# Kernel optimization log

Hardware: AMD Instinct MI355X
Metric: run time of the kernel (lower is better)

## Reference

```python
import jax, jax.numpy as jnp
import numpy as np


def _rgcn(x, src, dst, et, basis, comp, root, bias):
    # Basis-decomposed RGCNConv (PyG semantics): per-relation mean aggregation
    # over incoming edges + root transform + bias.
    N = x.shape[0]
    R = comp.shape[0]
    W = jnp.einsum('rb,bio->rio', comp, basis)          # [R, in, out]
    xr = jnp.einsum('ni,rio->rno', x, W)                 # [R, N, out]
    msg = xr[et, src]                                    # [E, out] gather per edge
    seg = dst * R + et                                   # (target, relation) segment id
    cnt = jax.ops.segment_sum(jnp.ones(et.shape, x.dtype), seg, num_segments=N * R)
    norm = 1.0 / jnp.maximum(cnt, 1.0)                   # mean per (dst, relation)
    msg = msg * norm[seg][:, None]
    agg = jax.ops.segment_sum(msg, dst, num_segments=N)  # scatter-add to targets
    return agg + x @ root + bias


def setup_inputs() -> dict:
    key = jax.random.key(0)
    ks = jax.random.split(key, 20)
    N, E, R, B, F, D, C, NB = 100000, 1600000, 5, 512, 4, 32, 5, 2
    s = 0.1
    inp = {
        'x': jax.random.normal(ks[0], (N, F), jnp.float32),
        'edge_index': jax.random.randint(ks[1], (2, E), 0, N, dtype=jnp.int32),
        'edge_type': jax.random.randint(ks[2], (E,), 0, R, dtype=jnp.int32),
        'start_nodes': jax.random.randint(ks[3], (B,), 0, N, dtype=jnp.int32),
        # layer 0: in=F, out=D
        'basis0': jax.random.normal(ks[4], (NB, F, D), jnp.float32) * s,
        'comp0': jax.random.normal(ks[5], (R, NB), jnp.float32) * s,
        'root0': jax.random.normal(ks[6], (F, D), jnp.float32) * s,
        'bias0': jax.random.normal(ks[7], (D,), jnp.float32) * s,
        # layers 1..3: in=out=D, stacked
        'basis': jax.random.normal(ks[8], (3, NB, D, D), jnp.float32) * s,
        'comp': jax.random.normal(ks[9], (3, R, NB), jnp.float32) * s,
        'root': jax.random.normal(ks[10], (3, D, D), jnp.float32) * s,
        'bias': jax.random.normal(ks[11], (3, D), jnp.float32) * s,
        # MLP head: sum(latent_dim)=128 -> 128 -> C
        'lin1_w': jax.random.normal(ks[12], (4 * D, 128), jnp.float32) * s,
        'lin1_b': jax.random.normal(ks[13], (128,), jnp.float32) * s,
        'lin2_w': jax.random.normal(ks[14], (128, C), jnp.float32) * s,
        'lin2_b': jax.random.normal(ks[15], (C,), jnp.float32) * s,
    }
    return inp


def reference(x, edge_index, edge_type, start_nodes, basis0, comp0, root0, bias0,
              basis, comp, root, bias, lin1_w, lin1_b, lin2_w, lin2_b):
    src, dst = edge_index[0], edge_index[1]
    h = jnp.tanh(_rgcn(x, src, dst, edge_type, basis0, comp0, root0, bias0))
    states = [h]
    for l in range(basis.shape[0]):
        h = jnp.tanh(_rgcn(h, src, dst, edge_type, basis[l], comp[l], root[l], bias[l]))
        states.append(h)
    concat = jnp.concatenate(states, axis=1)             # [N, 128]
    # Per-graph readout: the walk's degenerate n_walks=1 branch, i.e. the
    # start (user) node's concatenated state (sequential backtracking walk
    # replaced by its deterministic initialization path; eval mode, no dropout).
    acc = concat[start_nodes]                            # [B, 128]
    h1 = jax.nn.relu(acc @ lin1_w + lin1_b)
    logits = h1 @ lin2_w + lin2_b
    return jax.nn.log_softmax(logits, axis=-1)
```

## Files before the change

### kernel.cpp

```cpp
#include <hip/hip_runtime.h>
#include <cstdint>

#define N_NODES 100000
#define N_EDGES 1600000
#define R_REL   5
#define NBASIS  2
#define B_START 512
#define NBUCK   256
#define BUCK_SZ 391
#define EPB     6250
#define STAGE_CAP 7000

typedef __attribute__((ext_vector_type(8))) short short8;
typedef __attribute__((ext_vector_type(4))) float f32x4;
typedef _Float16 half8 __attribute__((ext_vector_type(8)));
typedef unsigned uint32x2 __attribute__((ext_vector_type(2)));
typedef unsigned uint32x4 __attribute__((ext_vector_type(4)));

__device__ __forceinline__ unsigned short f2bf(float f) {
    unsigned u = __float_as_uint(f);
    unsigned r = (u + 0x7FFF + ((u >> 16) & 1)) >> 16;
    return (unsigned short)r;
}
__device__ __forceinline__ float bf2f(unsigned short u) {
    return __uint_as_float(((unsigned)u) << 16);
}
__device__ __forceinline__ unsigned short f2h(float f) {
    _Float16 h = (_Float16)f;
    return __builtin_bit_cast(unsigned short, h);
}


__global__ __launch_bounds__(256) void k_cntb(
    const int* __restrict__ ei, int* __restrict__ bhist) {
    __shared__ int lh[NBUCK];
    int tid = threadIdx.x;
    lh[tid] = 0;
    __syncthreads();
    int base = blockIdx.x * EPB;
    for (int j = tid; j < EPB; j += 256) {
        int dst = ei[N_EDGES + base + j];
        atomicAdd(&lh[dst / BUCK_SZ], 1);
    }
    __syncthreads();
    bhist[blockIdx.x * NBUCK + tid] = lh[tid];
}

__global__ __launch_bounds__(256) void k_colscan(
    int* __restrict__ bhist, int* __restrict__ colsum) {
    __shared__ int s[256];
    int b = blockIdx.x, i = threadIdx.x;
    int v = bhist[i * NBUCK + b];
    s[i] = v;
    __syncthreads();
    for (int o = 1; o < 256; o <<= 1) {
        int t = (i >= o) ? s[i - o] : 0;
        __syncthreads();
        s[i] += t;
        __syncthreads();
    }
    bhist[i * NBUCK + b] = s[i] - v;
    if (i == 255) colsum[b] = s[255];
}

__global__ __launch_bounds__(256) void k_tiny(
    const int* __restrict__ colsum, int* __restrict__ bbase) {
    __shared__ int s[256];
    int i = threadIdx.x;
    int v = colsum[i];
    s[i] = v;
    __syncthreads();
    for (int o = 1; o < 256; o <<= 1) {
        int t = (i >= o) ? s[i - o] : 0;
        __syncthreads();
        s[i] += t;
        __syncthreads();
    }
    bbase[i] = s[i] - v;
    if (i == 255) bbase[NBUCK] = s[255];
}

__global__ __launch_bounds__(256) void k_scat(
    const int* __restrict__ ei, const int* __restrict__ et,
    const int* __restrict__ bhist, const int* __restrict__ bbase,
    int* __restrict__ arena) {
    __shared__ int lc[NBUCK];
    int tid = threadIdx.x;
    lc[tid] = bhist[blockIdx.x * NBUCK + tid] + bbase[tid];
    __syncthreads();
    int base = blockIdx.x * EPB;
    for (int j = tid; j < EPB; j += 256) {
        int e   = base + j;
        int src = ei[e];
        int dst = ei[N_EDGES + e];
        int t   = et[e];
        int bk  = dst / BUCK_SZ;
        int dl  = dst - bk * BUCK_SZ;
        int pos = atomicAdd(&lc[bk], 1);
        arena[pos] = src | (t << 17) | (dl << 20);
    }
}

__global__ __launch_bounds__(256) void k_build(
    const int* __restrict__ arena, const int* __restrict__ bbase,
    int* __restrict__ off, int* __restrict__ pk_m, float* __restrict__ nv5,
    unsigned* __restrict__ degpk) {
    __shared__ int deg5[BUCK_SZ * R_REL];
    __shared__ int loff[BUCK_SZ + 1];
    __shared__ int cur5[BUCK_SZ * R_REL];
    __shared__ int stg[STAGE_CAP];
    __shared__ int tsum[256];
    int b = blockIdx.x, tid = threadIdx.x;
    int base = bbase[b], end = bbase[b + 1];
    int count = end - base;
    for (int i = tid; i < BUCK_SZ * R_REL; i += 256) deg5[i] = 0;
    __syncthreads();
    for (int i = tid; i < count; i += 256) {
        int r  = arena[base + i];
        int dl = ((unsigned)r) >> 20;
        int t  = (r >> 17) & 7;
        atomicAdd(&deg5[dl * R_REL + t], 1);
    }
    __syncthreads();
    for (int dl = tid; dl < BUCK_SZ; dl += 256) {
        loff[dl] = deg5[dl * R_REL + 0] + deg5[dl * R_REL + 1] +
                   deg5[dl * R_REL + 2] + deg5[dl * R_REL + 3] +
                   deg5[dl * R_REL + 4];
    }
    __syncthreads();
    int d0 = 2 * tid, d1 = 2 * tid + 1;
    int va = (d0 < BUCK_SZ) ? loff[d0] : 0;
    int vb = (d1 < BUCK_SZ) ? loff[d1] : 0;
    tsum[tid] = va + vb;
    __syncthreads();
    for (int o = 1; o < 256; o <<= 1) {
        int v = (tid >= o) ? tsum[tid - o] : 0;
        __syncthreads();
        tsum[tid] += v;
        __syncthreads();
    }
    int pre = tsum[tid] - (va + vb);
    if (d0 < BUCK_SZ) loff[d0] = pre;
    if (d1 < BUCK_SZ) loff[d1] = pre + va;
    __syncthreads();
    for (int dl = tid; dl < BUCK_SZ; dl += 256) {
        int nn = b * BUCK_SZ + dl;
        int run = loff[dl];
        unsigned dp = 0;
#pragma unroll
        for (int t = 0; t < R_REL; t++) {
            cur5[dl * R_REL + t] = run;
            int c = deg5[dl * R_REL + t];
            run += c;
            int cc = c > 63 ? 63 : c;
            dp |= ((unsigned)cc) << (6 * t);
        }
        if (nn < N_NODES) {
            off[nn]   = base + loff[dl];
            degpk[nn] = dp;
#pragma unroll
            for (int t = 0; t < R_REL; t++) {
                int c = deg5[dl * R_REL + t];
                nv5[nn * R_REL + t] = 1.0f / (float)(c > 0 ? c : 1);
            }
        }
    }
    if (b == NBUCK - 1 && tid == 0) off[N_NODES] = N_EDGES;
    __syncthreads();
    for (int i = tid; i < count; i += 256) {
        int r  = arena[base + i];
        int dl = ((unsigned)r) >> 20;
        int t  = (r >> 17) & 7;
        int rk = atomicAdd(&cur5[dl * R_REL + t], 1);
        if (rk < STAGE_CAP) stg[rk] = r;
    }
    __syncthreads();
    for (int i = tid; i < count; i += 256) {
        int r = stg[i < STAGE_CAP ? i : STAGE_CAP - 1];
        pk_m[base + i] = r & 0x1FFFF;
    }
}


__global__ __launch_bounds__(256) void k_wprep(
    const float* __restrict__ basis, const float* __restrict__ comp,
    const float* __restrict__ root,  const float* __restrict__ basis0,
    const float* __restrict__ comp0, const float* __restrict__ root0,
    unsigned short* __restrict__ wfh, unsigned short* __restrict__ wfr,
    unsigned short* __restrict__ wf0) {
    __shared__ float lw[5120];
    int tid = threadIdx.x;
    int l = blockIdx.x;
    if (l < 3) {
        for (int idx = tid; idx < 5120; idx += 256) {
            int r = idx >> 10, rem = idx & 1023, i = rem >> 5, o = rem & 31;
            lw[idx] = comp[l * 10 + r * 2 + 0] * basis[l * 2048 + i * 32 + o]
                    + comp[l * 10 + r * 2 + 1] * basis[l * 2048 + 1024 + i * 32 + o];
        }
        __syncthreads();
        for (int idx = tid; idx < 5120; idx += 256) {
            int ot = idx / 2560, rem = idx % 2560;
            int s = rem >> 9, ln = (rem >> 3) & 63, j = idx & 7;
            int o = ot * 16 + (ln & 15), kk = (ln >> 4) * 8 + j;
            wfh[l * 5120 + idx] = f2h(lw[s * 1024 + kk * 32 + o]);
        }
        for (int idx = tid; idx < 2048; idx += 256) {
            int ot = idx >> 10, s = (idx >> 9) & 1, ln = (idx >> 3) & 63, j = idx & 7;
            int o = ot * 16 + (ln & 15), kk = (ln >> 4) * 8 + j;
            float val = root[l * 1024 + kk * 32 + o];
            unsigned short hi = f2bf(val);
            wfr[l * 2048 + idx] = s ? f2bf(val - bf2f(hi)) : hi;
        }
    } else {
        for (int idx = tid; idx < 1024; idx += 256) {
            int k = idx >> 5, o = idx & 31;
            float val = 0.f;
            if (k < 20) {
                int r = k >> 2, i = k & 3;
                val = comp0[r * 2 + 0] * basis0[i * 32 + o]
                    + comp0[r * 2 + 1] * basis0[128 + i * 32 + o];
            } else if (k < 24) val = root0[(k - 20) * 32 + o];
            lw[idx] = val;
        }
        __syncthreads();
        for (int idx = tid; idx < 1024; idx += 256) {
            int ot = idx >> 9, ln = (idx >> 3) & 63, j = idx & 7;
            int o = ot * 16 + (ln & 15), kk = (ln >> 4) * 8 + j;
            wf0[idx] = f2h(lw[kk * 32 + o]);
        }
    }
}


__global__ __launch_bounds__(256) void k_cvt0(
    const float* __restrict__ x, unsigned short* __restrict__ hb0) {
    int n = blockIdx.x * 256 + threadIdx.x;
    if (n >= N_NODES) return;
    float4 xv = *(const float4*)(x + (size_t)n * 4);
    unsigned short h0 = f2bf(xv.x), h1 = f2bf(xv.y), h2 = f2bf(xv.z), h3 = f2bf(xv.w);
    unsigned long long ph = (unsigned long long)h0 | ((unsigned long long)h1 << 16)
                          | ((unsigned long long)h2 << 32) | ((unsigned long long)h3 << 48);
    *(unsigned long long*)(hb0 + (size_t)n * 4) = ph;
}


__global__ __launch_bounds__(256) void k_gath32(
    const unsigned short* __restrict__ hb, const int* __restrict__ pk_m,
    const float* __restrict__ nv5, const unsigned* __restrict__ degpk,
    const int* __restrict__ off, unsigned short* __restrict__ agg) {
    int tid = threadIdx.x;
    int n = blockIdx.x * 8 + (tid >> 5);
    int lane32 = tid & 31;
    int s = lane32 >> 2;
    int cpos = lane32 & 3;

    int e0 = off[n];
    unsigned dp = degpk[n];
    int c0 = dp & 63, c1 = (dp >> 6) & 63, c2 = (dp >> 12) & 63,
        c3 = (dp >> 18) & 63, c4 = (dp >> 24) & 63;
    int cnt = s == 0 ? c0 : s == 1 ? c1 : s == 2 ? c2 : s == 3 ? c3
            : s == 4 ? c4 : 0;
    int start = (s > 0 ? c0 : 0) + (s > 1 ? c1 : 0) + (s > 2 ? c2 : 0)
              + (s > 3 ? c3 : 0);
    float nv = (s < R_REL) ? nv5[n * R_REL + s] : 0.f;

    const uint32x4* __restrict__ hb4 = (const uint32x4*)hb;
    float a0 = 0.f, a1 = 0.f, a2 = 0.f, a3 = 0.f;
    float a4 = 0.f, a5 = 0.f, a6 = 0.f, a7 = 0.f;
    int base = e0 + start;
    int pb = base < N_EDGES ? base : N_EDGES - 1;
    int mcur = __builtin_nontemporal_load(pk_m + pb);
    for (int k = 0; k < cnt; ++k) {
        int kn = k + 1 < cnt ? k + 1 : cnt - 1;
        int mnxt = __builtin_nontemporal_load(pk_m + base + kn);
        uint32x4 u = hb4[(size_t)mcur * 4 + cpos];
        a0 += nv * __uint_as_float(u.x << 16);
        a1 += nv * __uint_as_float(u.x & 0xFFFF0000u);
        a2 += nv * __uint_as_float(u.y << 16);
        a3 += nv * __uint_as_float(u.y & 0xFFFF0000u);
        a4 += nv * __uint_as_float(u.z << 16);
        a5 += nv * __uint_as_float(u.z & 0xFFFF0000u);
        a6 += nv * __uint_as_float(u.w << 16);
        a7 += nv * __uint_as_float(u.w & 0xFFFF0000u);
        mcur = mnxt;
    }
    if (s < R_REL) {
        uint32x4 pk;
        pk.x = (unsigned)f2h(a0) | ((unsigned)f2h(a1) << 16);
        pk.y = (unsigned)f2h(a2) | ((unsigned)f2h(a3) << 16);
        pk.z = (unsigned)f2h(a4) | ((unsigned)f2h(a5) << 16);
        pk.w = (unsigned)f2h(a6) | ((unsigned)f2h(a7) << 16);
        __builtin_nontemporal_store(pk,
            (uint32x4*)(agg + (size_t)n * 160 + s * 32 + cpos * 8));
    }
}


__global__ __launch_bounds__(256) void k_gath0(
    const unsigned short* __restrict__ hb0, const float* __restrict__ x,
    const int* __restrict__ pk_m, const float* __restrict__ nv5,
    const unsigned* __restrict__ degpk, const int* __restrict__ off,
    unsigned short* __restrict__ a0v) {
    int tid = threadIdx.x;
    int n = blockIdx.x * 32 + (tid >> 3);
    int s = tid & 7;

    int e0 = off[n];
    unsigned dp = degpk[n];
    int c0 = dp & 63, c1 = (dp >> 6) & 63, c2 = (dp >> 12) & 63,
        c3 = (dp >> 18) & 63, c4 = (dp >> 24) & 63;
    int cnt = s == 0 ? c0 : s == 1 ? c1 : s == 2 ? c2 : s == 3 ? c3
            : s == 4 ? c4 : 0;
    int start = (s > 0 ? c0 : 0) + (s > 1 ? c1 : 0) + (s > 2 ? c2 : 0)
              + (s > 3 ? c3 : 0);
    float nv = (s < R_REL) ? nv5[n * R_REL + s] : 0.f;

    const uint32x2* __restrict__ hb2 = (const uint32x2*)hb0;
    float a0 = 0.f, a1 = 0.f, a2 = 0.f, a3 = 0.f;
    int base = e0 + start;
    int pb = base < N_EDGES ? base : N_EDGES - 1;
    int mcur = __builtin_nontemporal_load(pk_m + pb);
    for (int k = 0; k < cnt; ++k) {
        int kn = k + 1 < cnt ? k + 1 : cnt - 1;
        int mnxt = __builtin_nontemporal_load(pk_m + base + kn);
        uint32x2 u = hb2[mcur];
        a0 += nv * __uint_as_float(u.x << 16);
        a1 += nv * __uint_as_float(u.x & 0xFFFF0000u);
        a2 += nv * __uint_as_float(u.y << 16);
        a3 += nv * __uint_as_float(u.y & 0xFFFF0000u);
        mcur = mnxt;
    }
    if (s < R_REL) {
        uint32x2 pk;
        pk.x = (unsigned)f2h(a0) | ((unsigned)f2h(a1) << 16);
        pk.y = (unsigned)f2h(a2) | ((unsigned)f2h(a3) << 16);
        __builtin_nontemporal_store(pk,
            (uint32x2*)(a0v + (size_t)n * 32 + s * 4));
    } else if (s == 5) {
        float4 xv = *(const float4*)(x + (size_t)n * 4);
        uint32x2 pk;
        pk.x = (unsigned)f2h(xv.x) | ((unsigned)f2h(xv.y) << 16);
        pk.y = (unsigned)f2h(xv.z) | ((unsigned)f2h(xv.w) << 16);
        __builtin_nontemporal_store(pk,
            (uint32x2*)(a0v + (size_t)n * 32 + 20));
    } else {
        uint32x2 z;
        z.x = 0u; z.y = 0u;
        __builtin_nontemporal_store(z,
            (uint32x2*)(a0v + (size_t)n * 32 + 24 + (s - 6) * 4));
    }
}


__global__ __launch_bounds__(256) void k_gemm(
    const unsigned short* __restrict__ agg, const unsigned short* __restrict__ hbin,
    const unsigned short* __restrict__ wfhl, const unsigned short* __restrict__ wfrl,
    const float* __restrict__ biasL, float* __restrict__ h,
    unsigned short* __restrict__ hbout) {
    int tid = threadIdx.x;
    int wid = tid >> 6, lane = tid & 63;
    int tile = blockIdx.x * 4 + wid;
    if (tile >= N_NODES / 16) return;
    int n0 = tile * 16;
    int row = lane & 15, kg = lane >> 4;
    const half8* ar = (const half8*)(agg + (size_t)(n0 + row) * 160 + kg * 8);
    const half8* wh = (const half8*)wfhl;
    const short8* wr = (const short8*)wfrl;
    short8 hbf = *(const short8*)(hbin + (size_t)(n0 + row) * 32 + kg * 8);
    f32x4 c0 = {0.f, 0.f, 0.f, 0.f}, c1 = {0.f, 0.f, 0.f, 0.f};
#pragma unroll
    for (int s = 0; s < 5; s++) {
        half8 a = __builtin_nontemporal_load(&ar[s * 4]);
        c0 = __builtin_amdgcn_mfma_f32_16x16x32_f16(a, wh[s * 64 + lane], c0, 0, 0, 0);
        c1 = __builtin_amdgcn_mfma_f32_16x16x32_f16(a, wh[320 + s * 64 + lane], c1, 0, 0, 0);
    }
    c0 = __builtin_amdgcn_mfma_f32_16x16x32_bf16(hbf, wr[lane], c0, 0, 0, 0);
    c0 = __builtin_amdgcn_mfma_f32_16x16x32_bf16(hbf, wr[64 + lane], c0, 0, 0, 0);
    c1 = __builtin_amdgcn_mfma_f32_16x16x32_bf16(hbf, wr[128 + lane], c1, 0, 0, 0);
    c1 = __builtin_amdgcn_mfma_f32_16x16x32_bf16(hbf, wr[192 + lane], c1, 0, 0, 0);
    float b0 = biasL[row], b1 = biasL[16 + row];
#pragma unroll
    for (int i = 0; i < 4; i++) {
        int n = n0 + kg * 4 + i;
        float t0 = tanhf(c0[i] + b0);
        float t1 = tanhf(c1[i] + b1);
        h[(size_t)n * 32 + row]      = t0;
        h[(size_t)n * 32 + 16 + row] = t1;
        hbout[(size_t)n * 32 + row]      = f2bf(t0);
        hbout[(size_t)n * 32 + 16 + row] = f2bf(t1);
    }
}

__global__ __launch_bounds__(256) void k_gemm0(
    const unsigned short* __restrict__ a0v, const unsigned short* __restrict__ wf0,
    const float* __restrict__ biasL, float* __restrict__ h,
    unsigned short* __restrict__ hbout) {
    int tid = threadIdx.x;
    int wid = tid >> 6, lane = tid & 63;
    int tile = blockIdx.x * 4 + wid;
    if (tile >= N_NODES / 16) return;
    int n0 = tile * 16;
    int row = lane & 15, kg = lane >> 4;
    half8 a = *(const half8*)(a0v + (size_t)(n0 + row) * 32 + kg * 8);
    const half8* wv = (const half8*)wf0;
    f32x4 c0 = {0.f, 0.f, 0.f, 0.f}, c1 = {0.f, 0.f, 0.f, 0.f};
    c0 = __builtin_amdgcn_mfma_f32_16x16x32_f16(a, wv[lane], c0, 0, 0, 0);
    c1 = __builtin_amdgcn_mfma_f32_16x16x32_f16(a, wv[64 + lane], c1, 0, 0, 0);
    float b0 = biasL[row], b1 = biasL[16 + row];
#pragma unroll
    for (int i = 0; i < 4; i++) {
        int n = n0 + kg * 4 + i;
        float t0 = tanhf(c0[i] + b0);
        float t1 = tanhf(c1[i] + b1);
        h[(size_t)n * 32 + row]      = t0;
        h[(size_t)n * 32 + 16 + row] = t1;
        hbout[(size_t)n * 32 + row]      = f2bf(t0);
        hbout[(size_t)n * 32 + 16 + row] = f2bf(t1);
    }
}


__global__ void k_save(const float* __restrict__ h, const int* __restrict__ start,
                       float* __restrict__ sav) {
    int t = blockIdx.x * blockDim.x + threadIdx.x;
    if (t < B_START * 32) {
        int b = t >> 5, ln = t & 31;
        sav[t] = h[(size_t)start[b] * 32 + ln];
    }
}

__global__ __launch_bounds__(128) void k_mlp(
    const float* __restrict__ sav, const float* __restrict__ w1,
    const float* __restrict__ b1, const float* __restrict__ w2,
    const float* __restrict__ b2, float* __restrict__ out) {
    __shared__ float cvec[128];
    __shared__ float hb[128];
    __shared__ float lg[8];
    int b = blockIdx.x, t = threadIdx.x;
    cvec[t] = sav[(t >> 5) * (B_START * 32) + b * 32 + (t & 31)];
    __syncthreads();
    float a = b1[t];
#pragma unroll 8
    for (int k = 0; k < 128; k++) a += cvec[k] * w1[k * 128 + t];
    hb[t] = fmaxf(a, 0.f);
    __syncthreads();
    if (t < 5) {
        float a2 = b2[t];
        for (int k = 0; k < 128; k++) a2 += hb[k] * w2[k * 5 + t];
        lg[t] = a2;
    }
    __syncthreads();
    if (t < 5) {
        float m = lg[0];
        for (int j = 1; j < 5; j++) m = fmaxf(m, lg[j]);
        float s = 0.f;
        for (int j = 0; j < 5; j++) s += expf(lg[j] - m);
        out[b * 5 + t] = lg[t] - m - logf(s);
    }
}


extern "C" void kernel_launch(void* const* d_in, const int* in_sizes, int n_in,
                              void* d_out, int out_size, void* d_ws, size_t ws_size,
                              hipStream_t stream) {
    const float* x      = (const float*)d_in[0];
    const int*   ei     = (const int*)d_in[1];
    const int*   etype  = (const int*)d_in[2];
    const int*   start  = (const int*)d_in[3];
    const float* basis0 = (const float*)d_in[4];
    const float* comp0  = (const float*)d_in[5];
    const float* root0  = (const float*)d_in[6];
    const float* bias0  = (const float*)d_in[7];
    const float* basis  = (const float*)d_in[8];
    const float* comp   = (const float*)d_in[9];
    const float* root   = (const float*)d_in[10];
    const float* bias   = (const float*)d_in[11];
    const float* w1     = (const float*)d_in[12];
    const float* b1     = (const float*)d_in[13];
    const float* w2     = (const float*)d_in[14];
    const float* b2     = (const float*)d_in[15];
    float* out = (float*)d_out;

    char* p = (char*)d_ws;
    auto alloc = [&](size_t bytes) -> void* {
        void* r = (void*)p;
        p += (bytes + 255) & ~(size_t)255;
        return r;
    };
    int*            bhist  = (int*)alloc((size_t)NBUCK * NBUCK * 4);
    int*            colsum = (int*)alloc(NBUCK * 4);
    int*            bbase  = (int*)alloc((NBUCK + 1) * 4);
    int*            arena  = (int*)alloc((size_t)N_EDGES * 4);
    int*            off    = (int*)alloc((N_NODES + 1) * 4);
    int*            pk_m   = (int*)alloc((size_t)N_EDGES * 4);
    float*          nv5    = (float*)alloc((size_t)N_NODES * R_REL * 4);
    unsigned*       degpk  = (unsigned*)alloc((size_t)N_NODES * 4);
    float*          h      = (float*)alloc((size_t)N_NODES * 32 * 4);
    unsigned short* hbuf   = (unsigned short*)alloc((size_t)(N_NODES + 64) * 32 * 2);
    unsigned short* hb0    = (unsigned short*)alloc((size_t)N_NODES * 4 * 2);
    unsigned short* a0v    = (unsigned short*)alloc((size_t)(N_NODES + 64) * 32 * 2);
    unsigned short* agg    = (unsigned short*)alloc((size_t)(N_NODES + 64) * 160 * 2);
    unsigned short* wfh    = (unsigned short*)alloc((size_t)3 * 5120 * 2);
    unsigned short* wfr    = (unsigned short*)alloc((size_t)3 * 2048 * 2);
    unsigned short* wf0    = (unsigned short*)alloc((size_t)1024 * 2);
    float*          sav    = (float*)alloc(4 * B_START * 32 * 4);

    k_cntb<<<NBUCK, 256, 0, stream>>>(ei, bhist);
    k_colscan<<<NBUCK, 256, 0, stream>>>(bhist, colsum);
    k_tiny<<<1, 256, 0, stream>>>(colsum, bbase);
    k_scat<<<NBUCK, 256, 0, stream>>>(ei, etype, bhist, bbase, arena);
    k_build<<<NBUCK, 256, 0, stream>>>(arena, bbase, off, pk_m, nv5, degpk);
    k_wprep<<<4, 256, 0, stream>>>(basis, comp, root, basis0, comp0, root0,
                                   wfh, wfr, wf0);
    k_cvt0<<<(N_NODES + 255) / 256, 256, 0, stream>>>(x, hb0);

    int nbGemm = (N_NODES / 16 + 3) / 4;

    k_gath0<<<N_NODES / 32, 256, 0, stream>>>(hb0, x, pk_m, nv5, degpk, off, a0v);
    k_gemm0<<<nbGemm, 256, 0, stream>>>(a0v, wf0, bias0, h, hbuf);
    k_save<<<64, 256, 0, stream>>>(h, start, sav);
    for (int l = 0; l < 3; l++) {
        k_gath32<<<N_NODES / 8, 256, 0, stream>>>(hbuf, pk_m, nv5, degpk, off, agg);
        k_gemm<<<nbGemm, 256, 0, stream>>>(agg, hbuf, wfh + (size_t)l * 5120,
                                           wfr + (size_t)l * 2048, bias + l * 32,
                                           h, hbuf);
        k_save<<<64, 256, 0, stream>>>(h, start, sav + (l + 1) * 16384);
    }

    k_mlp<<<B_START, 128, 0, stream>>>(sav, w1, b1, w2, b2, out);
}
```

Baseline: 407.0 us.

## Remap gather kernels to loop relations per thread with 4-way unrolled edge loads

Both gather kernels change their thread mapping. Layer 0 goes from 8 lanes per node, each owning one relation slot, to one thread per node that loops over all 5 relations. The 32-wide layers go from 32 lanes per node to 8 lanes per node, each lane owning 8 bytes of the feature row. Each thread now walks the relations in sequence and unrolls the edge loop by 4, issuing four index loads and four feature loads before the arithmetic. The aim is to stop wasting the idle relation lanes (s>=5) and to expose more memory-level parallelism per thread. The trade-off is longer serial per-thread work and narrower per-lane loads.

```diff
diff --git a/kernel.cpp b/kernel.cpp
--- a/kernel.cpp
+++ b/kernel.cpp
@@ -15,7 +15,6 @@
 typedef __attribute__((ext_vector_type(4))) float f32x4;
 typedef _Float16 half8 __attribute__((ext_vector_type(8)));
 typedef unsigned uint32x2 __attribute__((ext_vector_type(2)));
-typedef unsigned uint32x4 __attribute__((ext_vector_type(4)));
 
 __device__ __forceinline__ unsigned short f2bf(float f) {
     unsigned u = __float_as_uint(f);
@@ -249,49 +248,55 @@
     const float* __restrict__ nv5, const unsigned* __restrict__ degpk,
     const int* __restrict__ off, unsigned short* __restrict__ agg) {
     int tid = threadIdx.x;
-    int n = blockIdx.x * 8 + (tid >> 5);
-    int lane32 = tid & 31;
-    int s = lane32 >> 2;
-    int cpos = lane32 & 3;
-
-    int e0 = off[n];
+    int n = blockIdx.x * 32 + (tid >> 3);
+    int cpos = tid & 7;
+    const uint32x2* __restrict__ hb2 = (const uint32x2*)hb;
+
+    int e = off[n];
     unsigned dp = degpk[n];
-    int c0 = dp & 63, c1 = (dp >> 6) & 63, c2 = (dp >> 12) & 63,
-        c3 = (dp >> 18) & 63, c4 = (dp >> 24) & 63;
-    int cnt = s == 0 ? c0 : s == 1 ? c1 : s == 2 ? c2 : s == 3 ? c3
-            : s == 4 ? c4 : 0;
-    int start = (s > 0 ? c0 : 0) + (s > 1 ? c1 : 0) + (s > 2 ? c2 : 0)
-              + (s > 3 ? c3 : 0);
-    float nv = (s < R_REL) ? nv5[n * R_REL + s] : 0.f;
-
-    const uint32x4* __restrict__ hb4 = (const uint32x4*)hb;
-    float a0 = 0.f, a1 = 0.f, a2 = 0.f, a3 = 0.f;
-    float a4 = 0.f, a5 = 0.f, a6 = 0.f, a7 = 0.f;
-    int base = e0 + start;
-    int pb = base < N_EDGES ? base : N_EDGES - 1;
-    int mcur = __builtin_nontemporal_load(pk_m + pb);
-    for (int k = 0; k < cnt; ++k) {
-        int kn = k + 1 < cnt ? k + 1 : cnt - 1;
-        int mnxt = __builtin_nontemporal_load(pk_m + base + kn);
-        uint32x4 u = hb4[(size_t)mcur * 4 + cpos];
-        a0 += nv * __uint_as_float(u.x << 16);
-        a1 += nv * __uint_as_float(u.x & 0xFFFF0000u);
-        a2 += nv * __uint_as_float(u.y << 16);
-        a3 += nv * __uint_as_float(u.y & 0xFFFF0000u);
-        a4 += nv * __uint_as_float(u.z << 16);
-        a5 += nv * __uint_as_float(u.z & 0xFFFF0000u);
-        a6 += nv * __uint_as_float(u.w << 16);
-        a7 += nv * __uint_as_float(u.w & 0xFFFF0000u);
-        mcur = mnxt;
-    }
-    if (s < R_REL) {
-        uint32x4 pk;
+#pragma unroll
+    for (int r = 0; r < R_REL; r++) {
+        int cnt = (int)((dp >> (6 * r)) & 63u);
+        float nv = nv5[n * R_REL + r];
+        float a0 = 0.f, a1 = 0.f, a2 = 0.f, a3 = 0.f;
+        for (int kb = 0; kb < cnt; kb += 4) {
+            int i1 = kb + 1 < cnt ? kb + 1 : cnt - 1;
+            int i2 = kb + 2 < cnt ? kb + 2 : cnt - 1;
+            int i3 = kb + 3 < cnt ? kb + 3 : cnt - 1;
+            int m0 = __builtin_nontemporal_load(pk_m + e + kb);
+            int m1 = __builtin_nontemporal_load(pk_m + e + i1);
+            int m2 = __builtin_nontemporal_load(pk_m + e + i2);
+            int m3 = __builtin_nontemporal_load(pk_m + e + i3);
+            uint32x2 u0 = hb2[(size_t)m0 * 8 + cpos];
+            uint32x2 u1 = hb2[(size_t)m1 * 8 + cpos];
+            uint32x2 u2 = hb2[(size_t)m2 * 8 + cpos];
+            uint32x2 u3 = hb2[(size_t)m3 * 8 + cpos];
+            float w1 = (kb + 1 < cnt) ? nv : 0.f;
+            float w2 = (kb + 2 < cnt) ? nv : 0.f;
+            float w3 = (kb + 3 < cnt) ? nv : 0.f;
+            a0 += nv * __uint_as_float(u0.x << 16);
+            a1 += nv * __uint_as_float(u0.x & 0xFFFF0000u);
+            a2 += nv * __uint_as_float(u0.y << 16);
+            a3 += nv * __uint_as_float(u0.y & 0xFFFF0000u);
+            a0 += w1 * __uint_as_float(u1.x << 16);
+            a1 += w1 * __uint_as_float(u1.x & 0xFFFF0000u);
+            a2 += w1 * __uint_as_float(u1.y << 16);
+            a3 += w1 * __uint_as_float(u1.y & 0xFFFF0000u);
+            a0 += w2 * __uint_as_float(u2.x << 16);
+            a1 += w2 * __uint_as_float(u2.x & 0xFFFF0000u);
+            a2 += w2 * __uint_as_float(u2.y << 16);
+            a3 += w2 * __uint_as_float(u2.y & 0xFFFF0000u);
+            a0 += w3 * __uint_as_float(u3.x << 16);
+            a1 += w3 * __uint_as_float(u3.x & 0xFFFF0000u);
+            a2 += w3 * __uint_as_float(u3.y << 16);
+            a3 += w3 * __uint_as_float(u3.y & 0xFFFF0000u);
+        }
+        e += cnt;
+        uint32x2 pk;
         pk.x = (unsigned)f2h(a0) | ((unsigned)f2h(a1) << 16);
         pk.y = (unsigned)f2h(a2) | ((unsigned)f2h(a3) << 16);
-        pk.z = (unsigned)f2h(a4) | ((unsigned)f2h(a5) << 16);
-        pk.w = (unsigned)f2h(a6) | ((unsigned)f2h(a7) << 16);
         __builtin_nontemporal_store(pk,
-            (uint32x4*)(agg + (size_t)n * 160 + s * 32 + cpos * 8));
+            (uint32x2*)(agg + (size_t)n * 160 + r * 32 + cpos * 4));
     }
 }
 
@@ -301,54 +306,57 @@
     const int* __restrict__ pk_m, const float* __restrict__ nv5,
     const unsigned* __restrict__ degpk, const int* __restrict__ off,
     unsigned short* __restrict__ a0v) {
-    int tid = threadIdx.x;
-    int n = blockIdx.x * 32 + (tid >> 3);
-    int s = tid & 7;
-
-    int e0 = off[n];
+    int n = blockIdx.x * 256 + threadIdx.x;
+    if (n >= N_NODES) return;
+    const uint32x2* __restrict__ hb2 = (const uint32x2*)hb0;
+
+    int e = off[n];
     unsigned dp = degpk[n];
-    int c0 = dp & 63, c1 = (dp >> 6) & 63, c2 = (dp >> 12) & 63,
-        c3 = (dp >> 18) & 63, c4 = (dp >> 24) & 63;
-    int cnt = s == 0 ? c0 : s == 1 ? c1 : s == 2 ? c2 : s == 3 ? c3
-            : s == 4 ? c4 : 0;
-    int start = (s > 0 ? c0 : 0) + (s > 1 ? c1 : 0) + (s > 2 ? c2 : 0)
-              + (s > 3 ? c3 : 0);
-    float nv = (s < R_REL) ? nv5[n * R_REL + s] : 0.f;
-
-    const uint32x2* __restrict__ hb2 = (const uint32x2*)hb0;
-    float a0 = 0.f, a1 = 0.f, a2 = 0.f, a3 = 0.f;
-    int base = e0 + start;
-    int pb = base < N_EDGES ? base : N_EDGES - 1;
-    int mcur = __builtin_nontemporal_load(pk_m + pb);
-    for (int k = 0; k < cnt; ++k) {
-        int kn = k + 1 < cnt ? k + 1 : cnt - 1;
-        int mnxt = __builtin_nontemporal_load(pk_m + base + kn);
-        uint32x2 u = hb2[mcur];
-        a0 += nv * __uint_as_float(u.x << 16);
-        a1 += nv * __uint_as_float(u.x & 0xFFFF0000u);
-        a2 += nv * __uint_as_float(u.y << 16);
-        a3 += nv * __uint_as_float(u.y & 0xFFFF0000u);
-        mcur = mnxt;
-    }
-    if (s < R_REL) {
+#pragma unroll
+    for (int r = 0; r < R_REL; r++) {
+        int cnt = (int)((dp >> (6 * r)) & 63u);
+        float nv = nv5[n * R_REL + r];
+        float a0 = 0.f, a1 = 0.f, a2 = 0.f, a3 = 0.f;
+        for (int kb = 0; kb < cnt; kb += 4) {
+            int i1 = kb + 1 < cnt ? kb + 1 : cnt - 1;
+            int i2 = kb + 2 < cnt ? kb + 2 : cnt - 1;
+            int i3 = kb + 3 < cnt ? kb + 3 : cnt - 1;
+            int m0 = __builtin_nontemporal_load(pk_m + e + kb);
+            int m1 = __builtin_nontemporal_load(pk_m + e + i1);
+            int m2 = __builtin_nontemporal_load(pk_m + e + i2);
+            int m3 = __builtin_nontemporal_load(pk_m + e + i3);
+            uint32x2 u0 = hb2[m0];
+            uint32x2 u1 = hb2[m1];
+            uint32x2 u2 = hb2[m2];
+            uint32x2 u3 = hb2[m3];
+            float w1 = (kb + 1 < cnt) ? nv : 0.f;
+            float w2 = (kb + 2 < cnt) ? nv : 0.f;
+            float w3 = (kb + 3 < cnt) ? nv : 0.f;
+            a0 += nv * __uint_as_float(u0.x << 16) + w1 * __uint_as_float(u1.x << 16)
+                + w2 * __uint_as_float(u2.x << 16) + w3 * __uint_as_float(u3.x << 16);
+            a1 += nv * __uint_as_float(u0.x & 0xFFFF0000u) + w1 * __uint_as_float(u1.x & 0xFFFF0000u)
+                + w2 * __uint_as_float(u2.x & 0xFFFF0000u) + w3 * __uint_as_float(u3.x & 0xFFFF0000u);
+            a2 += nv * __uint_as_float(u0.y << 16) + w1 * __uint_as_float(u1.y << 16)
+                + w2 * __uint_as_float(u2.y << 16) + w3 * __uint_as_float(u3.y << 16);
+            a3 += nv * __uint_as_float(u0.y & 0xFFFF0000u) + w1 * __uint_as_float(u1.y & 0xFFFF0000u)
+                + w2 * __uint_as_float(u2.y & 0xFFFF0000u) + w3 * __uint_as_float(u3.y & 0xFFFF0000u);
+        }
+        e += cnt;
         uint32x2 pk;
         pk.x = (unsigned)f2h(a0) | ((unsigned)f2h(a1) << 16);
         pk.y = (unsigned)f2h(a2) | ((unsigned)f2h(a3) << 16);
         __builtin_nontemporal_store(pk,
-            (uint32x2*)(a0v + (size_t)n * 32 + s * 4));
-    } else if (s == 5) {
-        float4 xv = *(const float4*)(x + (size_t)n * 4);
-        uint32x2 pk;
-        pk.x = (unsigned)f2h(xv.x) | ((unsigned)f2h(xv.y) << 16);
-        pk.y = (unsigned)f2h(xv.z) | ((unsigned)f2h(xv.w) << 16);
-        __builtin_nontemporal_store(pk,
-            (uint32x2*)(a0v + (size_t)n * 32 + 20));
-    } else {
-        uint32x2 z;
-        z.x = 0u; z.y = 0u;
-        __builtin_nontemporal_store(z,
-            (uint32x2*)(a0v + (size_t)n * 32 + 24 + (s - 6) * 4));
-    }
+            (uint32x2*)(a0v + (size_t)n * 32 + r * 4));
+    }
+    float4 xv = *(const float4*)(x + (size_t)n * 4);
+    uint32x2 px;
+    px.x = (unsigned)f2h(xv.x) | ((unsigned)f2h(xv.y) << 16);
+    px.y = (unsigned)f2h(xv.z) | ((unsigned)f2h(xv.w) << 16);
+    __builtin_nontemporal_store(px, (uint32x2*)(a0v + (size_t)n * 32 + 20));
+    uint32x2 z;
+    z.x = 0u; z.y = 0u;
+    __builtin_nontemporal_store(z, (uint32x2*)(a0v + (size_t)n * 32 + 24));
+    __builtin_nontemporal_store(z, (uint32x2*)(a0v + (size_t)n * 32 + 28));
 }
 
 
@@ -516,11 +524,11 @@
 
     int nbGemm = (N_NODES / 16 + 3) / 4;
 
-    k_gath0<<<N_NODES / 32, 256, 0, stream>>>(hb0, x, pk_m, nv5, degpk, off, a0v);
+    k_gath0<<<(N_NODES + 255) / 256, 256, 0, stream>>>(hb0, x, pk_m, nv5, degpk, off, a0v);
     k_gemm0<<<nbGemm, 256, 0, stream>>>(a0v, wf0, bias0, h, hbuf);
     k_save<<<64, 256, 0, stream>>>(h, start, sav);
     for (int l = 0; l < 3; l++) {
-        k_gath32<<<N_NODES / 8, 256, 0, stream>>>(hbuf, pk_m, nv5, degpk, off, agg);
+        k_gath32<<<N_NODES / 32, 256, 0, stream>>>(hbuf, pk_m, nv5, degpk, off, agg);
         k_gemm<<<nbGemm, 256, 0, stream>>>(agg, hbuf, wfh + (size_t)l * 5120,
                                            wfr + (size_t)l * 2048, bias + l * 32,
                                            h, hbuf);
```

New measurement: 399.1 us. Within noise of the previous version (-1.9%).
